# Kernel tuning notes

Measured on AMD Instinct MI355X. Metric: run time of the kernel, lower is better.

The kernel has to match this reference:

```python
import jax, jax.numpy as jnp
import numpy as np

N_NODES = 100000
N_EDGES = 3200000
IN_DIM, HID_DIM, OUT_DIM = 256, 128, 64


def setup_inputs() -> dict:
    key = jax.random.key(0)
    ks = jax.random.split(key, 8)
    x = jax.random.normal(ks[0], (N_NODES, IN_DIM), dtype=jnp.float32)
    edge_index = jax.random.randint(ks[1], (2, N_EDGES), 0, N_NODES, dtype=jnp.int64)
    s = 0.05
    return {
        "x": x,
        "edge_index": edge_index,
        "W1": jax.random.normal(ks[2], (IN_DIM, HID_DIM), dtype=jnp.float32) * s,
        "b1": jnp.zeros((HID_DIM,), dtype=jnp.float32),
        "W2": jax.random.normal(ks[3], (HID_DIM, HID_DIM), dtype=jnp.float32) * s,
        "b2": jnp.zeros((HID_DIM,), dtype=jnp.float32),
        "W3": jax.random.normal(ks[4], (HID_DIM, OUT_DIM), dtype=jnp.float32) * s,
        "b3": jnp.zeros((OUT_DIM,), dtype=jnp.float32),
    }


def _gcn_conv(x, src, dst, deg_inv_sqrt, W, b):
    """PyG GCNConv: D^-1/2 (A+I) D^-1/2 (X W) + b.
    src/dst already include self-loops; deg_inv_sqrt precomputed per node."""
    h = x @ W  # [N, F_out] - transform first (smaller message dim)
    norm = deg_inv_sqrt[src] * deg_inv_sqrt[dst]  # [E]
    msg = h[src] * norm[:, None]  # gather + scale
    out = jax.ops.segment_sum(msg, dst, num_segments=x.shape[0])  # scatter-add
    return out + b


def reference(x, edge_index, W1, b1, W2, b2, W3, b3):
    n = x.shape[0]
    loops = jnp.arange(n, dtype=edge_index.dtype)
    src = jnp.concatenate([edge_index[0], loops])
    dst = jnp.concatenate([edge_index[1], loops])
    # symmetric normalization degree over (A + I), counted on dst as in PyG
    deg = jax.ops.segment_sum(jnp.ones_like(dst, dtype=x.dtype), dst, num_segments=n)
    deg_inv_sqrt = jnp.where(deg > 0, jax.lax.rsqrt(deg), 0.0)

    h = _gcn_conv(x, src, dst, deg_inv_sqrt, W1, b1)
    h = jax.nn.relu(h)  # dropout in eval mode = identity
    h = _gcn_conv(h, src, dst, deg_inv_sqrt, W2, b2)
    h = jax.nn.relu(h)
    h = _gcn_conv(h, src, dst, deg_inv_sqrt, W3, b3)
    return h
```

## Files before the change

### kernel.cpp

```cpp
#include <hip/hip_runtime.h>
#include <hip/hip_fp16.h>

constexpr int IN_DIM  = 256;
constexpr int HID_DIM = 128;
constexpr int OUT_DIM = 64;

constexpr int NPB_SHIFT = 8;
constexpr int NPB   = 1 << NPB_SHIFT;
constexpr int NBMAX = 512;
constexpr int CHUNK = 4096;
constexpr int CAP_B = 12288;

typedef _Float16 half8 __attribute__((ext_vector_type(8)));
typedef float floatx4 __attribute__((ext_vector_type(4)));


__global__ __launch_bounds__(256) void k_zero(int* __restrict__ p, int n) {
  int i = blockIdx.x * 256 + threadIdx.x;
  if (i < n) p[i] = 0;
}


__global__ __launch_bounds__(256) void k_hist(const int* __restrict__ dst, int E, int NB,
                                              int* __restrict__ bsize) {
  __shared__ int h[NBMAX];
  for (int i = threadIdx.x; i < NB; i += 256) h[i] = 0;
  __syncthreads();
  int e0 = blockIdx.x * CHUNK;
  int e1 = min(e0 + CHUNK, E);
  for (int e = e0 + threadIdx.x; e < e1; e += 256) {
    int d = __builtin_nontemporal_load(&dst[e]);
    atomicAdd(&h[d >> NPB_SHIFT], 1);
  }
  __syncthreads();
  for (int b = threadIdx.x; b < NB; b += 256) {
    int c = h[b];
    if (c) atomicAdd(&bsize[b], c);
  }
}

__global__ __launch_bounds__(512) void k_scanb(const int* __restrict__ bsize, int NB, int E,
                                               int* __restrict__ boff, int* __restrict__ gcur) {
  __shared__ int sh[NBMAX + 1];
  for (int i = threadIdx.x; i < NB; i += 512) sh[i] = bsize[i];
  __syncthreads();
  if (threadIdx.x == 0) {
    int run = 0;
    for (int b = 0; b < NB; b++) { int v = sh[b]; sh[b] = run; run += v; }
    sh[NB] = run;
  }
  __syncthreads();
  for (int i = threadIdx.x; i < NB; i += 512) { boff[i] = sh[i]; gcur[i] = sh[i]; }
  if (threadIdx.x == 0) boff[NB] = sh[NB];
}

__global__ __launch_bounds__(256) void k_binA(const int* __restrict__ src,
                                              const int* __restrict__ dst, int E, int NB,
                                              int* __restrict__ gcur,
                                              unsigned long long* __restrict__ bin) {
  __shared__ unsigned long long sbuf[CHUNK];
  __shared__ int h[NBMAX], lofs[NBMAX], wofs[NBMAX], hcur[NBMAX];
  for (int i = threadIdx.x; i < NB; i += 256) h[i] = 0;
  __syncthreads();
  int e0 = blockIdx.x * CHUNK;
  int e1 = min(e0 + CHUNK, E);
  for (int e = e0 + threadIdx.x; e < e1; e += 256) {
    int d = __builtin_nontemporal_load(&dst[e]);
    atomicAdd(&h[d >> NPB_SHIFT], 1);
  }
  __syncthreads();
  for (int b = threadIdx.x; b < NB; b += 256) {
    int c = h[b];
    if (c) wofs[b] = atomicAdd(&gcur[b], c);
  }
  if (threadIdx.x == 0) {
    int run = 0;
    for (int b = 0; b < NB; b++) { lofs[b] = run; run += h[b]; }
  }
  __syncthreads();
  for (int b = threadIdx.x; b < NB; b += 256) hcur[b] = lofs[b];
  __syncthreads();
  for (int e = e0 + threadIdx.x; e < e1; e += 256) {
    int d = dst[e];
    int s = src[e];
    int b = d >> NPB_SHIFT;
    int p = atomicAdd(&hcur[b], 1);
    sbuf[p] = ((unsigned long long)(unsigned)d << 32) | (unsigned)s;
  }
  __syncthreads();
  int total = e1 - e0;
  for (int i = threadIdx.x; i < total; i += 256) {
    unsigned long long v = sbuf[i];
    int b = (int)(v >> 32) >> NPB_SHIFT;
    bin[(size_t)wofs[b] + (i - lofs[b])] = v;
  }
}

__global__ __launch_bounds__(256) void k_passB(const unsigned long long* __restrict__ bin,
                                               const int* __restrict__ boff, int NB, int N, int E,
                                               int* __restrict__ rowptr, float* __restrict__ dis,
                                               int* __restrict__ col) {
  __shared__ unsigned int colbuf[CAP_B];
  __shared__ int lcnt[NPB], lofs2[NPB + 1], lpos[NPB];
  int b = blockIdx.x;
  int lo = b << NPB_SHIFT;
  int e0 = boff[b], e1 = boff[b + 1];
  int tot = e1 - e0;
  if (threadIdx.x < NPB) lcnt[threadIdx.x] = 0;
  __syncthreads();
  for (int i = threadIdx.x; i < tot; i += 256) {
    unsigned long long v = bin[(size_t)e0 + i];
    atomicAdd(&lcnt[(int)(v >> 32) & (NPB - 1)], 1);
  }
  __syncthreads();
  if (threadIdx.x == 0) {
    int run = 0;
    for (int i = 0; i < NPB; i++) { lofs2[i] = run; run += lcnt[i]; }
    lofs2[NPB] = run;
  }
  __syncthreads();
  if (threadIdx.x < NPB) {
    int node = lo + threadIdx.x;
    if (node < N) {
      rowptr[node] = e0 + lofs2[threadIdx.x];
      dis[node] = rsqrtf((float)lcnt[threadIdx.x] + 1.0f);
    }
    lpos[threadIdx.x] = lofs2[threadIdx.x];
  }
  __syncthreads();
  for (int i = threadIdx.x; i < tot; i += 256) {
    unsigned long long v = bin[(size_t)e0 + i];
    int idx = (int)(v >> 32) & (NPB - 1);
    int p = atomicAdd(&lpos[idx], 1);
    unsigned int s = (unsigned int)v;
    if (p < CAP_B) colbuf[p] = s;
    else col[(size_t)e0 + p] = s;
  }
  __syncthreads();
  int cp = min(tot, CAP_B);
  for (int i = threadIdx.x; i < cp; i += 256)
    __builtin_nontemporal_store(colbuf[i], (unsigned int*)&col[(size_t)e0 + i]);
  if (b == 0 && threadIdx.x == 0) rowptr[N] = E;
}


template <int K, int N>
__global__ __launch_bounds__(256) void k_packW(const float* __restrict__ W,
                                               _Float16* __restrict__ Wp) {
  int idx = blockIdx.x * 256 + threadIdx.x;
  if (idx >= K * N) return;
  int k = idx / N, n = idx % N;
  int ct = n >> 4, ks = k >> 5, q = (k >> 3) & 3, j = k & 7;
  int lane = (n & 15) + (q << 4);
  Wp[((((size_t)ct * (K / 32) + ks) * 64 + lane) << 3) + j] = (_Float16)W[idx];
}


template <int K, int N, typename AT>
__global__ __launch_bounds__(256) void k_gemm_mfma(const AT* __restrict__ A,
                                                   const _Float16* __restrict__ Wp,
                                                   const float* __restrict__ dis,
                                                   __half* __restrict__ out, int M) {
  constexpr int CT = N / 16;
  constexpr int KS = K / 32;
  const int wave = threadIdx.x >> 6, lane = threadIdx.x & 63;
  const int q = lane >> 4, mlane = lane & 15;
  const int row0 = blockIdx.x * 64 + wave * 16;
  int arow = row0 + mlane;
  if (arow > M - 1) arow = M - 1;

  floatx4 acc[CT];
#pragma unroll
  for (int c = 0; c < CT; c++) acc[c] = (floatx4){0.f, 0.f, 0.f, 0.f};

#pragma unroll
  for (int ks = 0; ks < KS; ks++) {
    half8 a;
    if constexpr (sizeof(AT) == 4) {
      const float* ap = &A[(size_t)arow * K + ks * 32 + q * 8];
      float4 f0 = *(const float4*)ap;
      float4 f1 = *(const float4*)(ap + 4);
      a[0] = (_Float16)f0.x; a[1] = (_Float16)f0.y;
      a[2] = (_Float16)f0.z; a[3] = (_Float16)f0.w;
      a[4] = (_Float16)f1.x; a[5] = (_Float16)f1.y;
      a[6] = (_Float16)f1.z; a[7] = (_Float16)f1.w;
    } else {
      a = *(const half8*)&A[(size_t)arow * K + ks * 32 + q * 8];
    }
#pragma unroll
    for (int c = 0; c < CT; c++) {
      half8 b = *(const half8*)&Wp[((((size_t)c * KS) + ks) * 64 + lane) << 3];
      acc[c] = __builtin_amdgcn_mfma_f32_16x16x32_f16(a, b, acc[c], 0, 0, 0);
    }
  }

  float dv[4]; int orow[4];
#pragma unroll
  for (int r = 0; r < 4; r++) {
    orow[r] = row0 + q * 4 + r;
    dv[r] = (orow[r] < M) ? dis[orow[r]] : 0.f;
  }
#pragma unroll
  for (int c = 0; c < CT; c++) {
    int cl = c * 16 + mlane;
#pragma unroll
    for (int r = 0; r < 4; r++)
      if (orow[r] < M)
        out[(size_t)orow[r] * N + cl] = __float2half_rn(dv[r] * acc[c][r]);
  }
}


template <int F, bool RELU, typename HOUT>
__global__ __launch_bounds__(256) void k_agg(const __half* __restrict__ g,
                                             const int* __restrict__ rowptr,
                                             const int* __restrict__ col,
                                             const float* __restrict__ dis,
                                             const float* __restrict__ bias,
                                             HOUT* __restrict__ out, int n) {
  int lane = threadIdx.x & 63;
  int v = blockIdx.x * 4 + (threadIdx.x >> 6);
  if (v >= n) return;
  int p = rowptr[v], end = rowptr[v + 1];
  float dv = dis[v];
  if (F == 128) {
    float2 f0 = __half22float2(*(const __half2*)&g[(size_t)v * 128 + lane * 2]);
    float ax = f0.x, ay = f0.y;
    for (; p + 8 <= end; p += 8) {
      int u[8];
#pragma unroll
      for (int j = 0; j < 8; j++) u[j] = __builtin_nontemporal_load(&col[p + j]);
      __half2 t[8];
#pragma unroll
      for (int j = 0; j < 8; j++) t[j] = *(const __half2*)&g[(size_t)u[j] * 128 + lane * 2];
#pragma unroll
      for (int j = 0; j < 8; j++) {
        float2 f = __half22float2(t[j]);
        ax += f.x; ay += f.y;
      }
    }
    for (; p < end; p++) {
      int u = __builtin_nontemporal_load(&col[p]);
      float2 f = __half22float2(*(const __half2*)&g[(size_t)u * 128 + lane * 2]);
      ax += f.x; ay += f.y;
    }
    float ox = fmaf(dv, ax, bias[lane * 2]);
    float oy = fmaf(dv, ay, bias[lane * 2 + 1]);
    if (RELU) { ox = fmaxf(ox, 0.f); oy = fmaxf(oy, 0.f); }
    if constexpr (sizeof(HOUT) == 2) {
      *(__half2*)&out[(size_t)v * 128 + lane * 2] = __float22half2_rn(make_float2(ox, oy));
    } else {
      float2 o; o.x = ox; o.y = oy;
      *(float2*)&out[(size_t)v * 128 + lane * 2] = o;
    }
  } else {
    float acc = __half2float(g[(size_t)v * 64 + lane]);
    for (; p + 8 <= end; p += 8) {
      int u[8];
#pragma unroll
      for (int j = 0; j < 8; j++) u[j] = __builtin_nontemporal_load(&col[p + j]);
      __half t[8];
#pragma unroll
      for (int j = 0; j < 8; j++) t[j] = g[(size_t)u[j] * 64 + lane];
#pragma unroll
      for (int j = 0; j < 8; j++) acc += __half2float(t[j]);
    }
    for (; p < end; p++) {
      int u = __builtin_nontemporal_load(&col[p]);
      acc += __half2float(g[(size_t)u * 64 + lane]);
    }
    float o = fmaf(dv, acc, bias[lane]);
    if (RELU) o = fmaxf(o, 0.f);
    out[(size_t)v * 64 + lane] = (HOUT)o;
  }
}


extern "C" void kernel_launch(void* const* d_in, const int* in_sizes, int n_in,
                              void* d_out, int out_size, void* d_ws, size_t ws_size,
                              hipStream_t stream) {
  const float* x  = (const float*)d_in[0];
  const int*   ei = (const int*)d_in[1];
  const float* W1 = (const float*)d_in[2];
  const float* b1 = (const float*)d_in[3];
  const float* W2 = (const float*)d_in[4];
  const float* b2 = (const float*)d_in[5];
  const float* W3 = (const float*)d_in[6];
  const float* b3 = (const float*)d_in[7];
  float* outp = (float*)d_out;

  const int N = in_sizes[0] / IN_DIM;
  const int E = in_sizes[1] / 2;
  const int* src = ei;
  const int* dst = ei + E;
  const int NB = (N + NPB - 1) >> NPB_SHIFT;

  char* w = (char*)d_ws;
  auto take = [&](size_t bytes) {
    char* r = w;
    w += (bytes + 255) & ~size_t(255);
    return r;
  };
  float*  dis    = (float*)take((size_t)N * 4);
  int*    rowptr = (int*)take((size_t)(N + 1) * 4);
  int*    bsize  = (int*)take((size_t)NB * 4);
  int*    boff   = (int*)take((size_t)(NB + 1) * 4);
  int*    gcur   = (int*)take((size_t)NB * 4);
  int*    col    = (int*)take((size_t)E * 4);
  unsigned long long* bin = (unsigned long long*)take((size_t)E * 8);
  _Float16* Wp1  = (_Float16*)take((size_t)IN_DIM * HID_DIM * 2);
  _Float16* Wp2  = (_Float16*)take((size_t)HID_DIM * HID_DIM * 2);
  _Float16* Wp3  = (_Float16*)take((size_t)HID_DIM * OUT_DIM * 2);
  __half* gbuf   = (__half*)take((size_t)N * 128 * 2);
  __half* bufH   = (__half*)take((size_t)N * 128 * 2);

  const int cb = (E + CHUNK - 1) / CHUNK;
  hipLaunchKernelGGL(k_zero, dim3((NB + 255) / 256), dim3(256), 0, stream, bsize, NB);
  hipLaunchKernelGGL(k_hist, dim3(cb), dim3(256), 0, stream, dst, E, NB, bsize);
  hipLaunchKernelGGL(k_scanb, dim3(1), dim3(512), 0, stream, bsize, NB, E, boff, gcur);
  hipLaunchKernelGGL(k_binA, dim3(cb), dim3(256), 0, stream, src, dst, E, NB, gcur, bin);
  hipLaunchKernelGGL(k_passB, dim3(NB), dim3(256), 0, stream, bin, boff, NB, N, E, rowptr, dis, col);

  hipLaunchKernelGGL((k_packW<IN_DIM, HID_DIM>), dim3((IN_DIM * HID_DIM + 255) / 256), dim3(256), 0, stream, W1, Wp1);
  hipLaunchKernelGGL((k_packW<HID_DIM, HID_DIM>), dim3((HID_DIM * HID_DIM + 255) / 256), dim3(256), 0, stream, W2, Wp2);
  hipLaunchKernelGGL((k_packW<HID_DIM, OUT_DIM>), dim3((HID_DIM * OUT_DIM + 255) / 256), dim3(256), 0, stream, W3, Wp3);

  const int gb = (N + 63) / 64;
  const int ab = (N + 3) / 4;
  hipLaunchKernelGGL((k_gemm_mfma<IN_DIM, HID_DIM, float>), dim3(gb), dim3(256), 0, stream, x, Wp1, dis, gbuf, N);
  hipLaunchKernelGGL((k_agg<128, true, __half>), dim3(ab), dim3(256), 0, stream, gbuf, rowptr, col, dis, b1, bufH, N);
  hipLaunchKernelGGL((k_gemm_mfma<HID_DIM, HID_DIM, __half>), dim3(gb), dim3(256), 0, stream, bufH, Wp2, dis, gbuf, N);
  hipLaunchKernelGGL((k_agg<128, true, __half>), dim3(ab), dim3(256), 0, stream, gbuf, rowptr, col, dis, b2, bufH, N);
  hipLaunchKernelGGL((k_gemm_mfma<HID_DIM, OUT_DIM, __half>), dim3(gb), dim3(256), 0, stream, bufH, Wp3, dis, gbuf, N);
  hipLaunchKernelGGL((k_agg<64, false, float>), dim3(ab), dim3(256), 0, stream, gbuf, rowptr, col, dis, b3, outp, N);
}
```

Before: 712.7 us.

## Store features in 16-column slices and pin slices to XCDs for aggregation

```diff
diff --git a/kernel.cpp b/kernel.cpp
--- a/kernel.cpp
+++ b/kernel.cpp
@@ -156,7 +156,7 @@
 }
 
 
-template <int K, int N, typename AT>
+template <int K, int N, typename AT, bool ASL>
 __global__ __launch_bounds__(256) void k_gemm_mfma(const AT* __restrict__ A,
                                                    const _Float16* __restrict__ Wp,
                                                    const float* __restrict__ dis,
@@ -184,6 +184,9 @@
       a[2] = (_Float16)f0.z; a[3] = (_Float16)f0.w;
       a[4] = (_Float16)f1.x; a[5] = (_Float16)f1.y;
       a[6] = (_Float16)f1.z; a[7] = (_Float16)f1.w;
+    } else if constexpr (ASL) {
+      const int sl = ks * 2 + (q >> 1);
+      a = *(const half8*)&A[((size_t)sl * M + arow) * 16 + (q & 1) * 8];
     } else {
       a = *(const half8*)&A[(size_t)arow * K + ks * 32 + q * 8];
     }
@@ -202,76 +205,81 @@
   }
 #pragma unroll
   for (int c = 0; c < CT; c++) {
-    int cl = c * 16 + mlane;
 #pragma unroll
     for (int r = 0; r < 4; r++)
       if (orow[r] < M)
-        out[(size_t)orow[r] * N + cl] = __float2half_rn(dv[r] * acc[c][r]);
-  }
-}
-
-
-template <int F, bool RELU, typename HOUT>
-__global__ __launch_bounds__(256) void k_agg(const __half* __restrict__ g,
-                                             const int* __restrict__ rowptr,
-                                             const int* __restrict__ col,
-                                             const float* __restrict__ dis,
-                                             const float* __restrict__ bias,
-                                             HOUT* __restrict__ out, int n) {
-  int lane = threadIdx.x & 63;
-  int v = blockIdx.x * 4 + (threadIdx.x >> 6);
-  if (v >= n) return;
+        out[((size_t)c * M + orow[r]) * 16 + mlane] = __float2half_rn(dv[r] * acc[c][r]);
+  }
+}
+
+
+template <int NS, bool RELU, typename OUT_T>
+__global__ __launch_bounds__(256) void k_agg_slice(const __half* __restrict__ g,
+                                                   const int* __restrict__ rowptr,
+                                                   const int* __restrict__ col,
+                                                   const float* __restrict__ dis,
+                                                   const float* __restrict__ bias,
+                                                   OUT_T* __restrict__ out, int n) {
+  constexpr int XPS = 8 / NS;
+  const int lane = threadIdx.x & 63;
+  const int sub  = lane >> 3;
+  const int li   = lane & 7;
+  const int wave = threadIdx.x >> 6;
+  const int bx   = blockIdx.x;
+  const int xcd  = bx & 7;
+  const int s    = xcd / XPS;
+  const int part = xcd % XPS;
+  const int nper = (n + XPS - 1) / XPS;
+  const int v0   = part * nper;
+  const int v1   = min(n, v0 + nper);
+  const int v    = v0 + ((bx >> 3) * 4 + wave) * 8 + sub;
+  if (v >= v1) return;
+
+  const __half2* __restrict__ gs = (const __half2*)g + (size_t)s * n * 8;
   int p = rowptr[v], end = rowptr[v + 1];
+  float2 acc = __half22float2(gs[(size_t)v * 8 + li]);
+
+  int rem = end - p;
+  while (rem >= 8) {
+    int u[8]; __half2 t[8];
+#pragma unroll
+    for (int j = 0; j < 8; j++) u[j] = __builtin_nontemporal_load(&col[p + j]);
+#pragma unroll
+    for (int j = 0; j < 8; j++) t[j] = gs[(size_t)u[j] * 8 + li];
+#pragma unroll
+    for (int j = 0; j < 8; j++) {
+      float2 f = __half22float2(t[j]);
+      acc.x += f.x; acc.y += f.y;
+    }
+    p += 8; rem -= 8;
+  }
+  if (rem > 0) {
+    int u[8]; __half2 t[8];
+#pragma unroll
+    for (int j = 0; j < 8; j++)
+      u[j] = __builtin_nontemporal_load(&col[(j < rem) ? p + j : p]);
+#pragma unroll
+    for (int j = 0; j < 8; j++) t[j] = gs[(size_t)u[j] * 8 + li];
+#pragma unroll
+    for (int j = 0; j < 8; j++) {
+      float2 f = __half22float2(t[j]);
+      if (j < rem) { acc.x += f.x; acc.y += f.y; }
+    }
+  }
+
   float dv = dis[v];
-  if (F == 128) {
-    float2 f0 = __half22float2(*(const __half2*)&g[(size_t)v * 128 + lane * 2]);
-    float ax = f0.x, ay = f0.y;
-    for (; p + 8 <= end; p += 8) {
-      int u[8];
-#pragma unroll
-      for (int j = 0; j < 8; j++) u[j] = __builtin_nontemporal_load(&col[p + j]);
-      __half2 t[8];
-#pragma unroll
-      for (int j = 0; j < 8; j++) t[j] = *(const __half2*)&g[(size_t)u[j] * 128 + lane * 2];
-#pragma unroll
-      for (int j = 0; j < 8; j++) {
-        float2 f = __half22float2(t[j]);
-        ax += f.x; ay += f.y;
-      }
-    }
-    for (; p < end; p++) {
-      int u = __builtin_nontemporal_load(&col[p]);
-      float2 f = __half22float2(*(const __half2*)&g[(size_t)u * 128 + lane * 2]);
-      ax += f.x; ay += f.y;
-    }
-    float ox = fmaf(dv, ax, bias[lane * 2]);
-    float oy = fmaf(dv, ay, bias[lane * 2 + 1]);
-    if (RELU) { ox = fmaxf(ox, 0.f); oy = fmaxf(oy, 0.f); }
-    if constexpr (sizeof(HOUT) == 2) {
-      *(__half2*)&out[(size_t)v * 128 + lane * 2] = __float22half2_rn(make_float2(ox, oy));
-    } else {
-      float2 o; o.x = ox; o.y = oy;
-      *(float2*)&out[(size_t)v * 128 + lane * 2] = o;
-    }
+  float2 bv = *(const float2*)&bias[s * 16 + li * 2];
+  float ox = fmaf(dv, acc.x, bv.x);
+  float oy = fmaf(dv, acc.y, bv.y);
+  if (RELU) { ox = fmaxf(ox, 0.f); oy = fmaxf(oy, 0.f); }
+  if constexpr (sizeof(OUT_T) == 2) {
+    __half2 h = __float22half2_rn(make_float2(ox, oy));
+    __builtin_nontemporal_store(*(const unsigned int*)&h,
+        (unsigned int*)&out[((size_t)s * n + v) * 16 + li * 2]);
   } else {
-    float acc = __half2float(g[(size_t)v * 64 + lane]);
-    for (; p + 8 <= end; p += 8) {
-      int u[8];
-#pragma unroll
-      for (int j = 0; j < 8; j++) u[j] = __builtin_nontemporal_load(&col[p + j]);
-      __half t[8];
-#pragma unroll
-      for (int j = 0; j < 8; j++) t[j] = g[(size_t)u[j] * 64 + lane];
-#pragma unroll
-      for (int j = 0; j < 8; j++) acc += __half2float(t[j]);
-    }
-    for (; p < end; p++) {
-      int u = __builtin_nontemporal_load(&col[p]);
-      acc += __half2float(g[(size_t)u * 64 + lane]);
-    }
-    float o = fmaf(dv, acc, bias[lane]);
-    if (RELU) o = fmaxf(o, 0.f);
-    out[(size_t)v * 64 + lane] = (HOUT)o;
+    float2 o = make_float2(ox, oy);
+    __builtin_nontemporal_store(*(const unsigned long long*)&o,
+        (unsigned long long*)&out[(size_t)v * (NS * 16) + s * 16 + li * 2]);
   }
 }
 
@@ -326,11 +334,18 @@
   hipLaunchKernelGGL((k_packW<HID_DIM, OUT_DIM>), dim3((HID_DIM * OUT_DIM + 255) / 256), dim3(256), 0, stream, W3, Wp3);
 
   const int gb = (N + 63) / 64;
-  const int ab = (N + 3) / 4;
-  hipLaunchKernelGGL((k_gemm_mfma<IN_DIM, HID_DIM, float>), dim3(gb), dim3(256), 0, stream, x, Wp1, dis, gbuf, N);
-  hipLaunchKernelGGL((k_agg<128, true, __half>), dim3(ab), dim3(256), 0, stream, gbuf, rowptr, col, dis, b1, bufH, N);
-  hipLaunchKernelGGL((k_gemm_mfma<HID_DIM, HID_DIM, __half>), dim3(gb), dim3(256), 0, stream, bufH, Wp2, dis, gbuf, N);
-  hipLaunchKernelGGL((k_agg<128, true, __half>), dim3(ab), dim3(256), 0, stream, gbuf, rowptr, col, dis, b2, bufH, N);
-  hipLaunchKernelGGL((k_gemm_mfma<HID_DIM, OUT_DIM, __half>), dim3(gb), dim3(256), 0, stream, bufH, Wp3, dis, gbuf, N);
-  hipLaunchKernelGGL((k_agg<64, false, float>), dim3(ab), dim3(256), 0, stream, gbuf, rowptr, col, dis, b3, outp, N);
-}
+  auto aggGrid = [&](int NSv) {
+    int xps = 8 / NSv;
+    int nper = (N + xps - 1) / xps;
+    return 8 * ((nper + 31) / 32);
+  };
+  const int ag8 = aggGrid(8);
+  const int ag4 = aggGrid(4);
+
+  hipLaunchKernelGGL((k_gemm_mfma<IN_DIM, HID_DIM, float, false>), dim3(gb), dim3(256), 0, stream, x, Wp1, dis, gbuf, N);
+  hipLaunchKernelGGL((k_agg_slice<8, true, __half>), dim3(ag8), dim3(256), 0, stream, gbuf, rowptr, col, dis, b1, bufH, N);
+  hipLaunchKernelGGL((k_gemm_mfma<HID_DIM, HID_DIM, __half, true>), dim3(gb), dim3(256), 0, stream, bufH, Wp2, dis, gbuf, N);
+  hipLaunchKernelGGL((k_agg_slice<8, true, __half>), dim3(ag8), dim3(256), 0, stream, gbuf, rowptr, col, dis, b2, bufH, N);
+  hipLaunchKernelGGL((k_gemm_mfma<HID_DIM, OUT_DIM, __half, true>), dim3(gb), dim3(256), 0, stream, bufH, Wp3, dis, gbuf, N);
+  hipLaunchKernelGGL((k_agg_slice<4, false, float>), dim3(ag4), dim3(256), 0, stream, gbuf, rowptr, col, dis, b3, outp, N);
+}
```

New measurement: 995.9 us. 1.4x slower.

## Split 128-wide aggregation into two column halves and pack bin entries to 32 bits

Applied to the files above, without the earlier changes.

```diff
diff --git a/kernel.cpp b/kernel.cpp
--- a/kernel.cpp
+++ b/kernel.cpp
@@ -15,12 +15,6 @@
 typedef float floatx4 __attribute__((ext_vector_type(4)));
 
 
-__global__ __launch_bounds__(256) void k_zero(int* __restrict__ p, int n) {
-  int i = blockIdx.x * 256 + threadIdx.x;
-  if (i < n) p[i] = 0;
-}
-
-
 __global__ __launch_bounds__(256) void k_hist(const int* __restrict__ dst, int E, int NB,
                                               int* __restrict__ bsize) {
   __shared__ int h[NBMAX];
@@ -57,8 +51,9 @@
 __global__ __launch_bounds__(256) void k_binA(const int* __restrict__ src,
                                               const int* __restrict__ dst, int E, int NB,
                                               int* __restrict__ gcur,
-                                              unsigned long long* __restrict__ bin) {
-  __shared__ unsigned long long sbuf[CHUNK];
+                                              unsigned int* __restrict__ bin) {
+  __shared__ unsigned int sbuf[CHUNK];
+  __shared__ unsigned short sbb[CHUNK];
   __shared__ int h[NBMAX], lofs[NBMAX], wofs[NBMAX], hcur[NBMAX];
   for (int i = threadIdx.x; i < NB; i += 256) h[i] = 0;
   __syncthreads();
@@ -85,18 +80,18 @@
     int s = src[e];
     int b = d >> NPB_SHIFT;
     int p = atomicAdd(&hcur[b], 1);
-    sbuf[p] = ((unsigned long long)(unsigned)d << 32) | (unsigned)s;
+    sbuf[p] = ((unsigned int)(d & (NPB - 1)) << 24) | (unsigned int)s;
+    sbb[p] = (unsigned short)b;
   }
   __syncthreads();
   int total = e1 - e0;
   for (int i = threadIdx.x; i < total; i += 256) {
-    unsigned long long v = sbuf[i];
-    int b = (int)(v >> 32) >> NPB_SHIFT;
-    bin[(size_t)wofs[b] + (i - lofs[b])] = v;
-  }
-}
-
-__global__ __launch_bounds__(256) void k_passB(const unsigned long long* __restrict__ bin,
+    int b = sbb[i];
+    bin[(size_t)wofs[b] + (i - lofs[b])] = sbuf[i];
+  }
+}
+
+__global__ __launch_bounds__(256) void k_passB(const unsigned int* __restrict__ bin,
                                                const int* __restrict__ boff, int NB, int N, int E,
                                                int* __restrict__ rowptr, float* __restrict__ dis,
                                                int* __restrict__ col) {
@@ -109,8 +104,8 @@
   if (threadIdx.x < NPB) lcnt[threadIdx.x] = 0;
   __syncthreads();
   for (int i = threadIdx.x; i < tot; i += 256) {
-    unsigned long long v = bin[(size_t)e0 + i];
-    atomicAdd(&lcnt[(int)(v >> 32) & (NPB - 1)], 1);
+    unsigned int v = bin[(size_t)e0 + i];
+    atomicAdd(&lcnt[v >> 24], 1);
   }
   __syncthreads();
   if (threadIdx.x == 0) {
@@ -129,12 +124,12 @@
   }
   __syncthreads();
   for (int i = threadIdx.x; i < tot; i += 256) {
-    unsigned long long v = bin[(size_t)e0 + i];
-    int idx = (int)(v >> 32) & (NPB - 1);
+    unsigned int v = bin[(size_t)e0 + i];
+    int idx = v >> 24;
     int p = atomicAdd(&lpos[idx], 1);
-    unsigned int s = (unsigned int)v;
+    unsigned int s = v & 0x00FFFFFFu;
     if (p < CAP_B) colbuf[p] = s;
-    else col[(size_t)e0 + p] = s;
+    else col[(size_t)e0 + p] = (int)s;
   }
   __syncthreads();
   int cp = min(tot, CAP_B);
@@ -145,14 +140,24 @@
 
 
 template <int K, int N>
-__global__ __launch_bounds__(256) void k_packW(const float* __restrict__ W,
-                                               _Float16* __restrict__ Wp) {
-  int idx = blockIdx.x * 256 + threadIdx.x;
-  if (idx >= K * N) return;
+__device__ inline void packW_one(const float* __restrict__ W, _Float16* __restrict__ Wp,
+                                 int idx) {
   int k = idx / N, n = idx % N;
   int ct = n >> 4, ks = k >> 5, q = (k >> 3) & 3, j = k & 7;
   int lane = (n & 15) + (q << 4);
   Wp[((((size_t)ct * (K / 32) + ks) * 64 + lane) << 3) + j] = (_Float16)W[idx];
+}
+
+__global__ __launch_bounds__(256) void k_packAll(const float* __restrict__ W1, _Float16* __restrict__ Wp1,
+                                                 const float* __restrict__ W2, _Float16* __restrict__ Wp2,
+                                                 const float* __restrict__ W3, _Float16* __restrict__ Wp3) {
+  constexpr int S1 = IN_DIM * HID_DIM;
+  constexpr int S2 = S1 + HID_DIM * HID_DIM;
+  constexpr int S3 = S2 + HID_DIM * OUT_DIM;
+  int idx = blockIdx.x * 256 + threadIdx.x;
+  if (idx < S1) packW_one<IN_DIM, HID_DIM>(W1, Wp1, idx);
+  else if (idx < S2) packW_one<HID_DIM, HID_DIM>(W2, Wp2, idx - S1);
+  else if (idx < S3) packW_one<HID_DIM, OUT_DIM>(W3, Wp3, idx - S2);
 }
 
 
@@ -211,68 +216,70 @@
 }
 
 
-template <int F, bool RELU, typename HOUT>
-__global__ __launch_bounds__(256) void k_agg(const __half* __restrict__ g,
-                                             const int* __restrict__ rowptr,
-                                             const int* __restrict__ col,
-                                             const float* __restrict__ dis,
-                                             const float* __restrict__ bias,
-                                             HOUT* __restrict__ out, int n) {
-  int lane = threadIdx.x & 63;
-  int v = blockIdx.x * 4 + (threadIdx.x >> 6);
+template <bool RELU>
+__global__ __launch_bounds__(256) void k_aggH(const __half* __restrict__ g,
+                                              const int* __restrict__ rowptr,
+                                              const int* __restrict__ col,
+                                              const float* __restrict__ dis,
+                                              const float* __restrict__ bias,
+                                              __half* __restrict__ out, int n, int hh) {
+  const int lane = threadIdx.x & 63;
+  const int v = blockIdx.x * 4 + (threadIdx.x >> 6);
   if (v >= n) return;
   int p = rowptr[v], end = rowptr[v + 1];
-  float dv = dis[v];
-  if (F == 128) {
-    float2 f0 = __half22float2(*(const __half2*)&g[(size_t)v * 128 + lane * 2]);
-    float ax = f0.x, ay = f0.y;
-    for (; p + 8 <= end; p += 8) {
-      int u[8];
-#pragma unroll
-      for (int j = 0; j < 8; j++) u[j] = __builtin_nontemporal_load(&col[p + j]);
-      __half2 t[8];
-#pragma unroll
-      for (int j = 0; j < 8; j++) t[j] = *(const __half2*)&g[(size_t)u[j] * 128 + lane * 2];
-#pragma unroll
-      for (int j = 0; j < 8; j++) {
-        float2 f = __half22float2(t[j]);
-        ax += f.x; ay += f.y;
-      }
-    }
-    for (; p < end; p++) {
-      int u = __builtin_nontemporal_load(&col[p]);
-      float2 f = __half22float2(*(const __half2*)&g[(size_t)u * 128 + lane * 2]);
-      ax += f.x; ay += f.y;
-    }
-    float ox = fmaf(dv, ax, bias[lane * 2]);
-    float oy = fmaf(dv, ay, bias[lane * 2 + 1]);
-    if (RELU) { ox = fmaxf(ox, 0.f); oy = fmaxf(oy, 0.f); }
-    if constexpr (sizeof(HOUT) == 2) {
-      *(__half2*)&out[(size_t)v * 128 + lane * 2] = __float22half2_rn(make_float2(ox, oy));
-    } else {
-      float2 o; o.x = ox; o.y = oy;
-      *(float2*)&out[(size_t)v * 128 + lane * 2] = o;
-    }
-  } else {
-    float acc = __half2float(g[(size_t)v * 64 + lane]);
-    for (; p + 8 <= end; p += 8) {
-      int u[8];
-#pragma unroll
-      for (int j = 0; j < 8; j++) u[j] = __builtin_nontemporal_load(&col[p + j]);
-      __half t[8];
-#pragma unroll
-      for (int j = 0; j < 8; j++) t[j] = g[(size_t)u[j] * 64 + lane];
-#pragma unroll
-      for (int j = 0; j < 8; j++) acc += __half2float(t[j]);
-    }
-    for (; p < end; p++) {
-      int u = __builtin_nontemporal_load(&col[p]);
-      acc += __half2float(g[(size_t)u * 64 + lane]);
-    }
-    float o = fmaf(dv, acc, bias[lane]);
-    if (RELU) o = fmaxf(o, 0.f);
-    out[(size_t)v * 64 + lane] = (HOUT)o;
-  }
+  const float dv = dis[v];
+  const __half* __restrict__ gh = g + hh * 64;
+
+  float acc = __half2float(gh[(size_t)v * 128 + lane]);
+  for (; p + 8 <= end; p += 8) {
+    int u[8];
+#pragma unroll
+    for (int j = 0; j < 8; j++) u[j] = __builtin_nontemporal_load(&col[p + j]);
+    __half t[8];
+#pragma unroll
+    for (int j = 0; j < 8; j++) t[j] = gh[(size_t)u[j] * 128 + lane];
+#pragma unroll
+    for (int j = 0; j < 8; j++) acc += __half2float(t[j]);
+  }
+  for (; p < end; p++) {
+    int u = __builtin_nontemporal_load(&col[p]);
+    acc += __half2float(gh[(size_t)u * 128 + lane]);
+  }
+  float o = fmaf(dv, acc, bias[hh * 64 + lane]);
+  if (RELU) o = fmaxf(o, 0.f);
+  out[(size_t)v * 128 + hh * 64 + lane] = __float2half_rn(o);
+}
+
+
+__global__ __launch_bounds__(256) void k_agg64(const __half* __restrict__ g,
+                                               const int* __restrict__ rowptr,
+                                               const int* __restrict__ col,
+                                               const float* __restrict__ dis,
+                                               const float* __restrict__ bias,
+                                               float* __restrict__ out, int n) {
+  const int lane = threadIdx.x & 63;
+  const int v = blockIdx.x * 4 + (threadIdx.x >> 6);
+  if (v >= n) return;
+  int p = rowptr[v], end = rowptr[v + 1];
+  const float dv = dis[v];
+
+  float acc = __half2float(g[(size_t)v * 64 + lane]);
+  for (; p + 8 <= end; p += 8) {
+    int u[8];
+#pragma unroll
+    for (int j = 0; j < 8; j++) u[j] = __builtin_nontemporal_load(&col[p + j]);
+    __half t[8];
+#pragma unroll
+    for (int j = 0; j < 8; j++) t[j] = g[(size_t)u[j] * 64 + lane];
+#pragma unroll
+    for (int j = 0; j < 8; j++) acc += __half2float(t[j]);
+  }
+  for (; p < end; p++) {
+    int u = __builtin_nontemporal_load(&col[p]);
+    acc += __half2float(g[(size_t)u * 64 + lane]);
+  }
+  float o = fmaf(dv, acc, bias[lane]);
+  out[(size_t)v * 64 + lane] = o;
 }
 
 
@@ -307,7 +314,7 @@
   int*    boff   = (int*)take((size_t)(NB + 1) * 4);
   int*    gcur   = (int*)take((size_t)NB * 4);
   int*    col    = (int*)take((size_t)E * 4);
-  unsigned long long* bin = (unsigned long long*)take((size_t)E * 8);
+  unsigned int* bin = (unsigned int*)take((size_t)E * 4);
   _Float16* Wp1  = (_Float16*)take((size_t)IN_DIM * HID_DIM * 2);
   _Float16* Wp2  = (_Float16*)take((size_t)HID_DIM * HID_DIM * 2);
   _Float16* Wp3  = (_Float16*)take((size_t)HID_DIM * OUT_DIM * 2);
@@ -315,22 +322,23 @@
   __half* bufH   = (__half*)take((size_t)N * 128 * 2);
 
   const int cb = (E + CHUNK - 1) / CHUNK;
-  hipLaunchKernelGGL(k_zero, dim3((NB + 255) / 256), dim3(256), 0, stream, bsize, NB);
+  hipMemsetAsync(bsize, 0, (size_t)NB * 4, stream);
   hipLaunchKernelGGL(k_hist, dim3(cb), dim3(256), 0, stream, dst, E, NB, bsize);
   hipLaunchKernelGGL(k_scanb, dim3(1), dim3(512), 0, stream, bsize, NB, E, boff, gcur);
   hipLaunchKernelGGL(k_binA, dim3(cb), dim3(256), 0, stream, src, dst, E, NB, gcur, bin);
   hipLaunchKernelGGL(k_passB, dim3(NB), dim3(256), 0, stream, bin, boff, NB, N, E, rowptr, dis, col);
 
-  hipLaunchKernelGGL((k_packW<IN_DIM, HID_DIM>), dim3((IN_DIM * HID_DIM + 255) / 256), dim3(256), 0, stream, W1, Wp1);
-  hipLaunchKernelGGL((k_packW<HID_DIM, HID_DIM>), dim3((HID_DIM * HID_DIM + 255) / 256), dim3(256), 0, stream, W2, Wp2);
-  hipLaunchKernelGGL((k_packW<HID_DIM, OUT_DIM>), dim3((HID_DIM * OUT_DIM + 255) / 256), dim3(256), 0, stream, W3, Wp3);
+  hipLaunchKernelGGL(k_packAll, dim3((IN_DIM * HID_DIM + HID_DIM * HID_DIM + HID_DIM * OUT_DIM + 255) / 256),
+                     dim3(256), 0, stream, W1, Wp1, W2, Wp2, W3, Wp3);
 
   const int gb = (N + 63) / 64;
   const int ab = (N + 3) / 4;
   hipLaunchKernelGGL((k_gemm_mfma<IN_DIM, HID_DIM, float>), dim3(gb), dim3(256), 0, stream, x, Wp1, dis, gbuf, N);
-  hipLaunchKernelGGL((k_agg<128, true, __half>), dim3(ab), dim3(256), 0, stream, gbuf, rowptr, col, dis, b1, bufH, N);
+  hipLaunchKernelGGL((k_aggH<true>), dim3(ab), dim3(256), 0, stream, gbuf, rowptr, col, dis, b1, bufH, N, 0);
+  hipLaunchKernelGGL((k_aggH<true>), dim3(ab), dim3(256), 0, stream, gbuf, rowptr, col, dis, b1, bufH, N, 1);
   hipLaunchKernelGGL((k_gemm_mfma<HID_DIM, HID_DIM, __half>), dim3(gb), dim3(256), 0, stream, bufH, Wp2, dis, gbuf, N);
-  hipLaunchKernelGGL((k_agg<128, true, __half>), dim3(ab), dim3(256), 0, stream, gbuf, rowptr, col, dis, b2, bufH, N);
+  hipLaunchKernelGGL((k_aggH<true>), dim3(ab), dim3(256), 0, stream, gbuf, rowptr, col, dis, b2, bufH, N, 0);
+  hipLaunchKernelGGL((k_aggH<true>), dim3(ab), dim3(256), 0, stream, gbuf, rowptr, col, dis, b2, bufH, N, 1);
   hipLaunchKernelGGL((k_gemm_mfma<HID_DIM, OUT_DIM, __half>), dim3(gb), dim3(256), 0, stream, bufH, Wp3, dis, gbuf, N);
-  hipLaunchKernelGGL((k_agg<64, false, float>), dim3(ab), dim3(256), 0, stream, gbuf, rowptr, col, dis, b3, outp, N);
-}
+  hipLaunchKernelGGL(k_agg64, dim3(ab), dim3(256), 0, stream, gbuf, rowptr, col, dis, b3, outp, N);
+}
```

Result: slower. 901.0 us (+26.4%).
